# Kernel optimization log

Measured on AMD Instinct MI355X. Metric: run time of the kernel, lower is better.

Reference implementation:

```python
import jax, jax.numpy as jnp
import numpy as np

H = 51  # hidden size hardcoded in the module
B, T, FUT = 4096, 512, 16


def setup_inputs() -> dict:
    key = jax.random.key(0)
    ks = jax.random.split(key, 12)
    s = 1.0 / np.sqrt(H)  # PyTorch default uniform init bound
    u = lambda k, shape: jax.random.uniform(k, shape, jnp.float32, -s, s)
    return {
        "input": jax.random.normal(ks[0], (B, T), jnp.float32),
        "W_ih1": u(ks[1], (4 * H, 1)),
        "W_hh1": u(ks[2], (4 * H, H)),
        "b_ih1": u(ks[3], (4 * H,)),
        "b_hh1": u(ks[4], (4 * H,)),
        "W_ih2": u(ks[5], (4 * H, H)),
        "W_hh2": u(ks[6], (4 * H, H)),
        "b_ih2": u(ks[7], (4 * H,)),
        "b_hh2": u(ks[8], (4 * H,)),
        "W_lin": u(ks[9], (1, H)),
        "b_lin": u(ks[10], (1,)),
        "future": FUT,
    }


def _cell(x, h, c, Wih, Whh, b):
    # PyTorch LSTMCell gate order: i, f, g, o
    g = x @ Wih.T + h @ Whh.T + b
    i, f, gg, o = jnp.split(g, 4, axis=-1)
    c = jax.nn.sigmoid(f) * c + jax.nn.sigmoid(i) * jnp.tanh(gg)
    h = jax.nn.sigmoid(o) * jnp.tanh(c)
    return h, c


def _forward(input, W_ih1, W_hh1, b_ih1, b_hh1, W_ih2, W_hh2, b_ih2, b_hh2, W_lin, b_lin, future):
    bsz = input.shape[0]
    dt = input.dtype
    b1 = b_ih1 + b_hh1
    b2 = b_ih2 + b_hh2
    z = jnp.zeros((bsz, H), dt)
    init = (z, z, z, z)

    def step(carry, x_t):
        h1, c1, h2, c2 = carry
        h1, c1 = _cell(x_t[:, None], h1, c1, W_ih1, W_hh1, b1)
        h2, c2 = _cell(h1, h2, c2, W_ih2, W_hh2, b2)
        out = h2 @ W_lin.T + b_lin  # [b, 1]
        return (h1, c1, h2, c2), out

    (h1, c1, h2, c2), outs = jax.lax.scan(step, init, input.T)  # outs: [t, b, 1]

    def fstep(carry, _):
        h1, c1, h2, c2, out = carry
        h1, c1 = _cell(out, h1, c1, W_ih1, W_hh1, b1)
        h2, c2 = _cell(h1, h2, c2, W_ih2, W_hh2, b2)
        out = h2 @ W_lin.T + b_lin
        return (h1, c1, h2, c2, out), out

    _, fouts = jax.lax.scan(fstep, (h1, c1, h2, c2, outs[-1]), None, length=future)
    all_outs = jnp.concatenate([outs, fouts], axis=0)  # [t+future, b, 1]
    return all_outs[..., 0].T  # [b, t+future]


def reference(input, W_ih1, W_hh1, b_ih1, b_hh1, W_ih2, W_hh2, b_ih2, b_hh2, W_lin, b_lin, future):
    return _forward(input, W_ih1, W_hh1, b_ih1, b_hh1, W_ih2, W_hh2, b_ih2, b_hh2, W_lin, b_lin, future)
```

## Files before the change

kernel.cpp:

```cpp
#include <hip/hip_runtime.h>

#define TSEQ 512
#define FUT  16
#define OT   (TSEQ + FUT)
#define NB   16
#define NWAVE 13
#define NTHREADS (NWAVE * 64)
#define OBS  20

typedef _Float16 f16x8 __attribute__((ext_vector_type(8)));
typedef float    f32x4 __attribute__((ext_vector_type(4)));

#define NL2E  (-1.44269504089f)
#define N2L2E (-2.88539008178f)

__device__ __forceinline__ f32x4 mfma16(f16x8 a, f16x8 b, f32x4 c) {
    return __builtin_amdgcn_mfma_f32_16x16x32_f16(a, b, c, 0, 0, 0);
}

__device__ __forceinline__ float exp2fast(float x) {
#if __has_builtin(__builtin_amdgcn_exp2f)
    return __builtin_amdgcn_exp2f(x);
#else
    float r;
    asm("v_exp_f32 %0, %1\n\ts_nop 1" : "=v"(r) : "v"(x));
    return r;
#endif
}

__device__ __forceinline__ float cell2(const f32x4 acc, float& c) {
    const float Ei = exp2fast(acc[0]);
    const float Ef = exp2fast(acc[1]);
    const float Eg = exp2fast(acc[2]);
    const float Eo = exp2fast(acc[3]);
    const float sf   = __builtin_amdgcn_rcpf(1.0f + Ef);
    const float sitg = (1.0f - Eg) * __builtin_amdgcn_rcpf((1.0f + Ei) * (1.0f + Eg));
    c = fmaf(sf, c, sitg);
    const float Ec = exp2fast(c * N2L2E);
    return (1.0f - Ec) * __builtin_amdgcn_rcpf((1.0f + Eo) * (1.0f + Ec));
}

__global__ __launch_bounds__(NTHREADS, 1) void lstm_mfma_kernel(
    const float* __restrict__ input,
    const float* __restrict__ W_ih1,
    const float* __restrict__ W_hh1,
    const float* __restrict__ b_ih1,
    const float* __restrict__ b_hh1,
    const float* __restrict__ W_ih2,
    const float* __restrict__ W_hh2,
    const float* __restrict__ b_ih2,
    const float* __restrict__ b_hh2,
    const float* __restrict__ W_lin,
    const float* __restrict__ b_lin,
    float* __restrict__ out)
{
    const int tid  = threadIdx.x;
    const int w    = tid >> 6;
    const int lane = tid & 63;
    const int n    = lane & 15;
    const int q    = lane >> 4;
    const int b0   = blockIdx.x * NB;

    __shared__ _Float16 H1[2][2][64][8] __attribute__((aligned(16)));
    __shared__ _Float16 H2[2][2][64][8] __attribute__((aligned(16)));
    __shared__ float OB[2][16][OBS] __attribute__((aligned(16)));

    const int ru  = 4 * w + (n >> 2);
    const bool rv = (ru < 51);
    const int R   = 51 * (n & 3) + (rv ? ru : 50);
    const bool olin_row = (w == 12) && (n == 12);
    const float rsc = ((n & 3) == 2) ? N2L2E : NL2E;

    f16x8 W1h[2], W1l[2], W2h[4], W2l[4];
#pragma unroll
    for (int s = 0; s < 2; ++s) {
#pragma unroll
        for (int e = 0; e < 8; ++e) {
            const int k = 32 * s + 8 * q + e;
            float wv = 0.0f;
            if (rv) {
                if (k < 51)       wv = rsc * W_hh1[R * 51 + k];
                else if (k == 51) wv = rsc * W_ih1[R];
            }
            const _Float16 hi = (_Float16)wv;
            W1h[s][e] = hi;
            W1l[s][e] = (_Float16)(wv - (float)hi);
        }
    }
#pragma unroll
    for (int s = 0; s < 4; ++s) {
#pragma unroll
        for (int e = 0; e < 8; ++e) {
            const int k = 32 * s + 8 * q + e;
            float wv = 0.0f;
            if (rv) {
                if (k < 51)                  wv = rsc * W_ih2[R * 51 + k];
                else if (k >= 64 && k < 115) wv = rsc * W_hh2[R * 51 + (k - 64)];
            } else if (olin_row) {
                if (k >= 64 && k < 115)      wv = W_lin[k - 64];
            }
            const _Float16 hi = (_Float16)wv;
            W2h[s][e] = hi;
            W2l[s][e] = (_Float16)(wv - (float)hi);
        }
    }

    const int uu = 4 * w + q;
    const bool ustore = (uu < 51);
    const bool oduty = (w == 12) && (q == 3);
    f32x4 bias1v, bias2v;
#pragma unroll
    for (int r = 0; r < 4; ++r) {
        const int row = 51 * r + (ustore ? uu : 50);
        const float s = (r == 2) ? N2L2E : NL2E;
        bias1v[r] = ustore ? s * (b_ih1[row] + b_hh1[row]) : 0.0f;
        bias2v[r] = ustore ? s * (b_ih2[row] + b_hh2[row]) : 0.0f;
    }
    const float blin = b_lin[0];
    if (oduty) bias2v[0] = blin;
    const float wlin = ustore ? W_lin[uu] : 0.0f;
    const int uuX = ustore ? uu : 60;
    const int us = uuX >> 5;
    const int lp = n + 16 * ((uuX & 31) >> 3);
    const int ue = uuX & 7;

    {
        const f16x8 zz = {0, 0, 0, 0, 0, 0, 0, 0};
        f16x8* p1 = (f16x8*)&H1[0][0][0][0];
        f16x8* p2 = (f16x8*)&H2[0][0][0][0];
        for (int i = tid; i < 2 * 2 * 64; i += NTHREADS) { p1[i] = zz; p2[i] = zz; }
    }
    __syncthreads();

    float c1 = 0.0f, c2 = 0.0f;

    f32x4 xv = {0, 0, 0, 0}, xvn = {0, 0, 0, 0};
    if (w == 12 && q == 2) {
        xv  = *(const f32x4*)&input[(b0 + n) * TSEQ + 0];
        xvn = *(const f32x4*)&input[(b0 + n) * TSEQ + 4];
    }

    f32x4 obuf = {0, 0, 0, 0};

    {
        f16x8 xk1 = {0,0,0,0,0,0,0,0};
        if (w == 12 && q == 2) {
            xk1[3] = (_Float16)xv[0];
            H1[1][1][32 + n][3] = (_Float16)xv[1];
        }
        float x0 = input[(b0 + n) * TSEQ + 0];
        f16x8 xf = {0,0,0,0,0,0,0,0};
        if (q == 2) xf[3] = (_Float16)x0;
        f32x4 a1 = mfma16(W1h[1], xf, bias1v);
        a1 = mfma16(W1l[1], xf, a1);
        const float h1n = cell2(a1, c1);
        H1[1][us][lp][ue] = (_Float16)h1n;
    }
    __syncthreads();

#define PHASE(t_, W_, ROT_, OSL_, OSTORE_, FLUSH_, LOADN_, XW_)                \
    {                                                                          \
        const int p_  = (t_) & 1;                                              \
        const int pn_ = p_ ^ 1;                                                \
        const f16x8 h1k0 = *(const f16x8*)&H1[p_][0][lane][0];                 \
        const f16x8 h1k1 = *(const f16x8*)&H1[p_][1][lane][0];                 \
        const f16x8 h2k0 = *(const f16x8*)&H2[p_][0][lane][0];                 \
        const f16x8 h2k1 = *(const f16x8*)&H2[p_][1][lane][0];                 \
        if (w == 12) {                                                         \
            if (ROT_) xv = xvn;                                                \
            if ((LOADN_) && q == 2)                                            \
                xvn = *(const f32x4*)&input[(b0 + n) * TSEQ + (t_) + 3];       \
            if ((XW_) && q == 2)                                               \
                H1[pn_][1][32 + n][3] = (_Float16)xv[W_];                      \
        }                                                                      \
        f32x4 a1 = mfma16(W1h[0], h1k0, bias1v);                               \
        a1 = mfma16(W1l[0], h1k0, a1);                                         \
        a1 = mfma16(W1h[1], h1k1, a1);                                         \
        a1 = mfma16(W1l[1], h1k1, a1);                                         \
        f32x4 a2 = mfma16(W2h[0], h1k0, bias2v);                               \
        a2 = mfma16(W2l[0], h1k0, a2);                                         \
        a2 = mfma16(W2h[1], h1k1, a2);                                         \
        a2 = mfma16(W2l[1], h1k1, a2);                                         \
        a2 = mfma16(W2h[2], h2k0, a2);                                         \
        a2 = mfma16(W2l[2], h2k0, a2);                                         \
        a2 = mfma16(W2h[3], h2k1, a2);                                         \
        a2 = mfma16(W2l[3], h2k1, a2);                                         \
        if (OSTORE_) obuf[OSL_] = a2[0];                                       \
        if ((FLUSH_) && oduty)                                                 \
            *reinterpret_cast<f32x4*>(&out[(b0 + n) * OT + (t_) - 5]) = obuf;  \
        const float h1n = cell2(a1, c1);                                       \
        const float h2n = cell2(a2, c2);                                       \
        H1[pn_][us][lp][ue] = (_Float16)h1n;                                   \
        H2[pn_][us][lp][ue] = (_Float16)h2n;                                   \
        __syncthreads();                                                       \
    }

    PHASE(  1,   2, 0,  0,  0,  0,  0,  1)
    for (int tb = 2; tb + 3 <= 505; tb += 4) {
        PHASE(tb + 0, 3, 0, 0, 1, 0, 0, 1)
        PHASE(tb + 1, 0, 1, 1, 1, 0, 0, 1)
        PHASE(tb + 2, 1, 0, 2, 1, 0, 0, 1)
        PHASE(tb + 3, 2, 0, 3, 1, 1, 1, 1)
    }
    PHASE(506, 3, 0, 0, 1, 0, 0, 1)
    PHASE(507, 0, 1, 1, 1, 0, 0, 1)
    PHASE(508, 1, 0, 2, 1, 0, 0, 1)
    PHASE(509, 2, 0, 3, 1, 1, 0, 1)
    PHASE(510, 3, 0, 0, 1, 0, 0, 1)
    PHASE(511, 0, 0, 1, 1, 0, 0, 0)
#undef PHASE

    if (oduty) {
        out[(b0 + n) * OT + 508] = obuf[0];
        out[(b0 + n) * OT + 509] = obuf[1];
    }

    for (int t = TSEQ; t < OT; ++t) {
        const int p  = t & 1;
        const int pn = p ^ 1;

        const f16x8 h1k0 = *(const f16x8*)&H1[p][0][lane][0];
        f16x8 h1k1       = *(const f16x8*)&H1[p][1][lane][0];
        const f16x8 h2k0 = *(const f16x8*)&H2[p][0][lane][0];
        const f16x8 h2k1 = *(const f16x8*)&H2[p][1][lane][0];
        f32x4 a2 = mfma16(W2h[0], h1k0, bias2v);
        a2 = mfma16(W2l[0], h1k0, a2);
        a2 = mfma16(W2h[1], h1k1, a2);
        a2 = mfma16(W2l[1], h1k1, a2);
        a2 = mfma16(W2h[2], h2k0, a2);
        a2 = mfma16(W2l[2], h2k0, a2);
        a2 = mfma16(W2h[3], h2k1, a2);
        a2 = mfma16(W2l[3], h2k1, a2);
        if (oduty && t == TSEQ) out[(b0 + n) * OT + (TSEQ - 2)] = a2[0];
        const float h2n = cell2(a2, c2);
        H2[pn][us][lp][ue] = (_Float16)h2n;
        float po = h2n * wlin;
        po += __shfl_xor(po, 16, 64);
        po += __shfl_xor(po, 32, 64);
        if (lane < 16) OB[p][lane][w] = po;
        __syncthreads();

        float xcur = 0.0f;
        if (q == 2) {
            const float* ob = &OB[p][n][0];
            const f32x4 s0 = *(const f32x4*)&ob[0];
            const f32x4 s1 = *(const f32x4*)&ob[4];
            const f32x4 s2 = *(const f32x4*)&ob[8];
            const float o = ((s0[0] + s0[1]) + (s0[2] + s0[3]))
                          + ((s1[0] + s1[1]) + (s1[2] + s1[3]))
                          + ((s2[0] + s2[1]) + (s2[2] + s2[3])) + ob[12] + blin;
            if (w == 0) out[(b0 + n) * OT + (t - 1)] = o;
            xcur = o;
        }
        if (q == 2) h1k1[3] = (_Float16)xcur;
        f32x4 a1 = mfma16(W1h[0], h1k0, bias1v);
        a1 = mfma16(W1l[0], h1k0, a1);
        a1 = mfma16(W1h[1], h1k1, a1);
        a1 = mfma16(W1l[1], h1k1, a1);
        const float h1n = cell2(a1, c1);
        H1[pn][us][lp][ue] = (_Float16)h1n;
        __syncthreads();
    }

    {
        const f16x8 h1k0 = *(const f16x8*)&H1[0][0][lane][0];
        const f16x8 h1k1 = *(const f16x8*)&H1[0][1][lane][0];
        const f16x8 h2k0 = *(const f16x8*)&H2[0][0][lane][0];
        const f16x8 h2k1 = *(const f16x8*)&H2[0][1][lane][0];
        f32x4 a2 = mfma16(W2h[0], h1k0, bias2v);
        a2 = mfma16(W2l[0], h1k0, a2);
        a2 = mfma16(W2h[1], h1k1, a2);
        a2 = mfma16(W2l[1], h1k1, a2);
        a2 = mfma16(W2h[2], h2k0, a2);
        a2 = mfma16(W2l[2], h2k0, a2);
        a2 = mfma16(W2h[3], h2k1, a2);
        a2 = mfma16(W2l[3], h2k1, a2);
        const float h2n = cell2(a2, c2);
        float po = h2n * wlin;
        po += __shfl_xor(po, 16, 64);
        po += __shfl_xor(po, 32, 64);
        if (lane < 16) OB[0][lane][w] = po;
        __syncthreads();
        if (w == 0 && lane < 16) {
            const float* ob = &OB[0][lane][0];
            const f32x4 s0 = *(const f32x4*)&ob[0];
            const f32x4 s1 = *(const f32x4*)&ob[4];
            const f32x4 s2 = *(const f32x4*)&ob[8];
            out[(b0 + lane) * OT + (OT - 1)] =
                ((s0[0] + s0[1]) + (s0[2] + s0[3])) +
                ((s1[0] + s1[1]) + (s1[2] + s1[3])) +
                ((s2[0] + s2[1]) + (s2[2] + s2[3])) + ob[12] + blin;
        }
    }
}

extern "C" void kernel_launch(void* const* d_in, const int* in_sizes, int n_in,
                              void* d_out, int out_size, void* d_ws, size_t ws_size,
                              hipStream_t stream) {
    const float* input = (const float*)d_in[0];
    const float* W_ih1 = (const float*)d_in[1];
    const float* W_hh1 = (const float*)d_in[2];
    const float* b_ih1 = (const float*)d_in[3];
    const float* b_hh1 = (const float*)d_in[4];
    const float* W_ih2 = (const float*)d_in[5];
    const float* W_hh2 = (const float*)d_in[6];
    const float* b_ih2 = (const float*)d_in[7];
    const float* b_hh2 = (const float*)d_in[8];
    const float* W_lin = (const float*)d_in[9];
    const float* b_lin = (const float*)d_in[10];

    const int bsz = in_sizes[0] / TSEQ;

    hipLaunchKernelGGL(lstm_mfma_kernel, dim3(bsz / NB), dim3(NTHREADS), 0, stream,
                       input, W_ih1, W_hh1, b_ih1, b_hh1,
                       W_ih2, W_hh2, b_ih2, b_hh2, W_lin, b_lin,
                       (float*)d_out);
}
```

Baseline: 417.5 us.

## Cut block to 7 waves, each computing two gate tiles, allow 2 blocks/CU

Reduces the workgroup from 13 to 7 waves, so six waves now compute two 4-unit gate tiles (A and B) and one computes a single tile. Launch bounds are raised to allow two blocks per CU. The aim is to cut barrier cost per step and raise occupancy so more batch blocks run at once. The trade-off is doubled register pressure for weights per wave, a longer serial MFMA chain per wave on each step, and load imbalance from the wave without a B tile.

Result: slower. 449.9 us (+7.7%).

```diff
diff --git a/kernel.cpp b/kernel.cpp
--- a/kernel.cpp
+++ b/kernel.cpp
@@ -4,7 +4,7 @@
 #define FUT  16
 #define OT   (TSEQ + FUT)
 #define NB   16
-#define NWAVE 13
+#define NWAVE 7
 #define NTHREADS (NWAVE * 64)
 #define OBS  20
 
@@ -40,7 +40,7 @@
     return (1.0f - Ec) * __builtin_amdgcn_rcpf((1.0f + Eo) * (1.0f + Ec));
 }
 
-__global__ __launch_bounds__(NTHREADS, 1) void lstm_mfma_kernel(
+__global__ __launch_bounds__(NTHREADS, 2) void lstm_mfma_kernel(
     const float* __restrict__ input,
     const float* __restrict__ W_ih1,
     const float* __restrict__ W_hh1,
@@ -61,68 +61,90 @@
     const int q    = lane >> 4;
     const int b0   = blockIdx.x * NB;
 
+    const int tA = w;
+    const int tB = w + 7;
+    const bool hasB = (w < 6);
+
     __shared__ _Float16 H1[2][2][64][8] __attribute__((aligned(16)));
     __shared__ _Float16 H2[2][2][64][8] __attribute__((aligned(16)));
     __shared__ float OB[2][16][OBS] __attribute__((aligned(16)));
 
-    const int ru  = 4 * w + (n >> 2);
-    const bool rv = (ru < 51);
-    const int R   = 51 * (n & 3) + (rv ? ru : 50);
-    const bool olin_row = (w == 12) && (n == 12);
     const float rsc = ((n & 3) == 2) ? N2L2E : NL2E;
 
-    f16x8 W1h[2], W1l[2], W2h[4], W2l[4];
-#pragma unroll
-    for (int s = 0; s < 2; ++s) {
-#pragma unroll
-        for (int e = 0; e < 8; ++e) {
-            const int k = 32 * s + 8 * q + e;
-            float wv = 0.0f;
-            if (rv) {
-                if (k < 51)       wv = rsc * W_hh1[R * 51 + k];
-                else if (k == 51) wv = rsc * W_ih1[R];
-            }
-            const _Float16 hi = (_Float16)wv;
-            W1h[s][e] = hi;
-            W1l[s][e] = (_Float16)(wv - (float)hi);
-        }
-    }
-#pragma unroll
-    for (int s = 0; s < 4; ++s) {
-#pragma unroll
-        for (int e = 0; e < 8; ++e) {
-            const int k = 32 * s + 8 * q + e;
-            float wv = 0.0f;
-            if (rv) {
-                if (k < 51)                  wv = rsc * W_ih2[R * 51 + k];
-                else if (k >= 64 && k < 115) wv = rsc * W_hh2[R * 51 + (k - 64)];
-            } else if (olin_row) {
-                if (k >= 64 && k < 115)      wv = W_lin[k - 64];
-            }
-            const _Float16 hi = (_Float16)wv;
-            W2h[s][e] = hi;
-            W2l[s][e] = (_Float16)(wv - (float)hi);
-        }
-    }
-
-    const int uu = 4 * w + q;
-    const bool ustore = (uu < 51);
-    const bool oduty = (w == 12) && (q == 3);
-    f32x4 bias1v, bias2v;
+    f16x8 W1hA[2], W1lA[2], W2hA[4], W2lA[4];
+    f16x8 W1hB[2], W1lB[2], W2hB[4], W2lB[4];
+
+#define LOADW(TT, W1h, W1l, W2h, W2l)                                          \
+    {                                                                          \
+        const int ru = 4 * (TT) + (n >> 2);                                    \
+        const bool rv = (ru < 51);                                             \
+        const int R = 51 * (n & 3) + (rv ? ru : 50);                           \
+        const bool olin = ((TT) == 12) && (n == 12);                           \
+        _Pragma("unroll")                                                      \
+        for (int s = 0; s < 2; ++s) {                                          \
+            _Pragma("unroll")                                                  \
+            for (int e = 0; e < 8; ++e) {                                      \
+                const int k = 32 * s + 8 * q + e;                              \
+                float wv = 0.0f;                                               \
+                if (rv) {                                                      \
+                    if (k < 51)       wv = rsc * W_hh1[R * 51 + k];            \
+                    else if (k == 51) wv = rsc * W_ih1[R];                     \
+                }                                                              \
+                const _Float16 hi = (_Float16)wv;                              \
+                W1h[s][e] = hi;                                                \
+                W1l[s][e] = (_Float16)(wv - (float)hi);                        \
+            }                                                                  \
+        }                                                                      \
+        _Pragma("unroll")                                                      \
+        for (int s = 0; s < 4; ++s) {                                          \
+            _Pragma("unroll")                                                  \
+            for (int e = 0; e < 8; ++e) {                                      \
+                const int k = 32 * s + 8 * q + e;                              \
+                float wv = 0.0f;                                               \
+                if (rv) {                                                      \
+                    if (k < 51)                  wv = rsc * W_ih2[R * 51 + k]; \
+                    else if (k >= 64 && k < 115) wv = rsc * W_hh2[R * 51 + (k - 64)]; \
+                } else if (olin) {                                             \
+                    if (k >= 64 && k < 115)      wv = W_lin[k - 64];           \
+                }                                                              \
+                const _Float16 hi = (_Float16)wv;                              \
+                W2h[s][e] = hi;                                                \
+                W2l[s][e] = (_Float16)(wv - (float)hi);                        \
+            }                                                                  \
+        }                                                                      \
+    }
+
+    LOADW(tA, W1hA, W1lA, W2hA, W2lA)
+    LOADW(tB, W1hB, W1lB, W2hB, W2lB)
+#undef LOADW
+
+    const int uuA = 4 * tA + q;
+    const int uuB = 4 * tB + q;
+    const bool ustA = (uuA < 51);
+    const bool ustB = (uuB < 51) && hasB;
+    const bool oduty = (w == 5) && (q == 3);
+    const float blin = b_lin[0];
+
+    f32x4 bias1A, bias2A, bias1B, bias2B;
 #pragma unroll
     for (int r = 0; r < 4; ++r) {
-        const int row = 51 * r + (ustore ? uu : 50);
         const float s = (r == 2) ? N2L2E : NL2E;
-        bias1v[r] = ustore ? s * (b_ih1[row] + b_hh1[row]) : 0.0f;
-        bias2v[r] = ustore ? s * (b_ih2[row] + b_hh2[row]) : 0.0f;
-    }
-    const float blin = b_lin[0];
-    if (oduty) bias2v[0] = blin;
-    const float wlin = ustore ? W_lin[uu] : 0.0f;
-    const int uuX = ustore ? uu : 60;
-    const int us = uuX >> 5;
-    const int lp = n + 16 * ((uuX & 31) >> 3);
-    const int ue = uuX & 7;
+        const int rowA = 51 * r + (ustA ? uuA : 50);
+        bias1A[r] = ustA ? s * (b_ih1[rowA] + b_hh1[rowA]) : 0.0f;
+        bias2A[r] = ustA ? s * (b_ih2[rowA] + b_hh2[rowA]) : 0.0f;
+        const int rowB = 51 * r + (ustB ? uuB : 50);
+        bias1B[r] = ustB ? s * (b_ih1[rowB] + b_hh1[rowB]) : 0.0f;
+        bias2B[r] = ustB ? s * (b_ih2[rowB] + b_hh2[rowB]) : 0.0f;
+    }
+    if (oduty) bias2B[0] = blin;
+
+    const float wlinA = ustA ? W_lin[uuA] : 0.0f;
+    const float wlinB = ustB ? W_lin[uuB] : 0.0f;
+
+    const int uuXA = ustA ? uuA : 60;
+    const int usA = uuXA >> 5, lpA = n + 16 * ((uuXA & 31) >> 3), ueA = uuXA & 7;
+    const int uuXB = ustB ? uuB : 60;
+    const int usB = uuXB >> 5, lpB = n + 16 * ((uuXB & 31) >> 3), ueB = uuXB & 7;
 
     {
         const f16x8 zz = {0, 0, 0, 0, 0, 0, 0, 0};
@@ -132,10 +154,10 @@
     }
     __syncthreads();
 
-    float c1 = 0.0f, c2 = 0.0f;
+    float c1A = 0.0f, c2A = 0.0f, c1B = 0.0f, c2B = 0.0f;
 
     f32x4 xv = {0, 0, 0, 0}, xvn = {0, 0, 0, 0};
-    if (w == 12 && q == 2) {
+    if (w == 6 && q == 2) {
         xv  = *(const f32x4*)&input[(b0 + n) * TSEQ + 0];
         xvn = *(const f32x4*)&input[(b0 + n) * TSEQ + 4];
     }
@@ -143,18 +165,20 @@
     f32x4 obuf = {0, 0, 0, 0};
 
     {
-        f16x8 xk1 = {0,0,0,0,0,0,0,0};
-        if (w == 12 && q == 2) {
-            xk1[3] = (_Float16)xv[0];
-            H1[1][1][32 + n][3] = (_Float16)xv[1];
-        }
-        float x0 = input[(b0 + n) * TSEQ + 0];
+        const float x0 = input[(b0 + n) * TSEQ + 0];
+        if (w == 6 && q == 2) H1[1][1][32 + n][3] = (_Float16)xv[1];
         f16x8 xf = {0,0,0,0,0,0,0,0};
         if (q == 2) xf[3] = (_Float16)x0;
-        f32x4 a1 = mfma16(W1h[1], xf, bias1v);
-        a1 = mfma16(W1l[1], xf, a1);
-        const float h1n = cell2(a1, c1);
-        H1[1][us][lp][ue] = (_Float16)h1n;
+        f32x4 a1 = mfma16(W1hA[1], xf, bias1A);
+        a1 = mfma16(W1lA[1], xf, a1);
+        const float h1A = cell2(a1, c1A);
+        H1[1][usA][lpA][ueA] = (_Float16)h1A;
+        if (hasB) {
+            f32x4 b1 = mfma16(W1hB[1], xf, bias1B);
+            b1 = mfma16(W1lB[1], xf, b1);
+            const float h1B = cell2(b1, c1B);
+            H1[1][usB][lpB][ueB] = (_Float16)h1B;
+        }
     }
     __syncthreads();
 
@@ -166,32 +190,50 @@
         const f16x8 h1k1 = *(const f16x8*)&H1[p_][1][lane][0];                 \
         const f16x8 h2k0 = *(const f16x8*)&H2[p_][0][lane][0];                 \
         const f16x8 h2k1 = *(const f16x8*)&H2[p_][1][lane][0];                 \
-        if (w == 12) {                                                         \
+        if (w == 6) {                                                          \
             if (ROT_) xv = xvn;                                                \
             if ((LOADN_) && q == 2)                                            \
                 xvn = *(const f32x4*)&input[(b0 + n) * TSEQ + (t_) + 3];       \
             if ((XW_) && q == 2)                                               \
                 H1[pn_][1][32 + n][3] = (_Float16)xv[W_];                      \
         }                                                                      \
-        f32x4 a1 = mfma16(W1h[0], h1k0, bias1v);                               \
-        a1 = mfma16(W1l[0], h1k0, a1);                                         \
-        a1 = mfma16(W1h[1], h1k1, a1);                                         \
-        a1 = mfma16(W1l[1], h1k1, a1);                                         \
-        f32x4 a2 = mfma16(W2h[0], h1k0, bias2v);                               \
-        a2 = mfma16(W2l[0], h1k0, a2);                                         \
-        a2 = mfma16(W2h[1], h1k1, a2);                                         \
-        a2 = mfma16(W2l[1], h1k1, a2);                                         \
-        a2 = mfma16(W2h[2], h2k0, a2);                                         \
-        a2 = mfma16(W2l[2], h2k0, a2);                                         \
-        a2 = mfma16(W2h[3], h2k1, a2);                                         \
-        a2 = mfma16(W2l[3], h2k1, a2);                                         \
-        if (OSTORE_) obuf[OSL_] = a2[0];                                       \
-        if ((FLUSH_) && oduty)                                                 \
-            *reinterpret_cast<f32x4*>(&out[(b0 + n) * OT + (t_) - 5]) = obuf;  \
-        const float h1n = cell2(a1, c1);                                       \
-        const float h2n = cell2(a2, c2);                                       \
-        H1[pn_][us][lp][ue] = (_Float16)h1n;                                   \
-        H2[pn_][us][lp][ue] = (_Float16)h2n;                                   \
+        f32x4 a1 = mfma16(W1hA[0], h1k0, bias1A);                              \
+        a1 = mfma16(W1lA[0], h1k0, a1);                                        \
+        a1 = mfma16(W1hA[1], h1k1, a1);                                        \
+        a1 = mfma16(W1lA[1], h1k1, a1);                                        \
+        f32x4 a2 = mfma16(W2hA[0], h1k0, bias2A);                              \
+        a2 = mfma16(W2lA[0], h1k0, a2);                                        \
+        a2 = mfma16(W2hA[1], h1k1, a2);                                        \
+        a2 = mfma16(W2lA[1], h1k1, a2);                                        \
+        a2 = mfma16(W2hA[2], h2k0, a2);                                        \
+        a2 = mfma16(W2lA[2], h2k0, a2);                                        \
+        a2 = mfma16(W2hA[3], h2k1, a2);                                        \
+        a2 = mfma16(W2lA[3], h2k1, a2);                                        \
+        const float h1nA = cell2(a1, c1A);                                     \
+        const float h2nA = cell2(a2, c2A);                                     \
+        H1[pn_][usA][lpA][ueA] = (_Float16)h1nA;                               \
+        H2[pn_][usA][lpA][ueA] = (_Float16)h2nA;                               \
+        if (hasB) {                                                            \
+            f32x4 b1 = mfma16(W1hB[0], h1k0, bias1B);                          \
+            b1 = mfma16(W1lB[0], h1k0, b1);                                    \
+            b1 = mfma16(W1hB[1], h1k1, b1);                                    \
+            b1 = mfma16(W1lB[1], h1k1, b1);                                    \
+            f32x4 b2 = mfma16(W2hB[0], h1k0, bias2B);                          \
+            b2 = mfma16(W2lB[0], h1k0, b2);                                    \
+            b2 = mfma16(W2hB[1], h1k1, b2);                                    \
+            b2 = mfma16(W2lB[1], h1k1, b2);                                    \
+            b2 = mfma16(W2hB[2], h2k0, b2);                                    \
+            b2 = mfma16(W2lB[2], h2k0, b2);                                    \
+            b2 = mfma16(W2hB[3], h2k1, b2);                                    \
+            b2 = mfma16(W2lB[3], h2k1, b2);                                    \
+            if (OSTORE_) obuf[OSL_] = b2[0];                                   \
+            if ((FLUSH_) && oduty)                                             \
+                *reinterpret_cast<f32x4*>(&out[(b0 + n) * OT + (t_) - 5]) = obuf; \
+            const float h1nB = cell2(b1, c1B);                                 \
+            const float h2nB = cell2(b2, c2B);                                 \
+            H1[pn_][usB][lpB][ueB] = (_Float16)h1nB;                           \
+            H2[pn_][usB][lpB][ueB] = (_Float16)h2nB;                           \
+        }                                                                      \
         __syncthreads();                                                       \
     }
 
@@ -223,21 +265,37 @@
         f16x8 h1k1       = *(const f16x8*)&H1[p][1][lane][0];
         const f16x8 h2k0 = *(const f16x8*)&H2[p][0][lane][0];
         const f16x8 h2k1 = *(const f16x8*)&H2[p][1][lane][0];
-        f32x4 a2 = mfma16(W2h[0], h1k0, bias2v);
-        a2 = mfma16(W2l[0], h1k0, a2);
-        a2 = mfma16(W2h[1], h1k1, a2);
-        a2 = mfma16(W2l[1], h1k1, a2);
-        a2 = mfma16(W2h[2], h2k0, a2);
-        a2 = mfma16(W2l[2], h2k0, a2);
-        a2 = mfma16(W2h[3], h2k1, a2);
-        a2 = mfma16(W2l[3], h2k1, a2);
-        if (oduty && t == TSEQ) out[(b0 + n) * OT + (TSEQ - 2)] = a2[0];
-        const float h2n = cell2(a2, c2);
-        H2[pn][us][lp][ue] = (_Float16)h2n;
-        float po = h2n * wlin;
-        po += __shfl_xor(po, 16, 64);
-        po += __shfl_xor(po, 32, 64);
-        if (lane < 16) OB[p][lane][w] = po;
+        f32x4 a2 = mfma16(W2hA[0], h1k0, bias2A);
+        a2 = mfma16(W2lA[0], h1k0, a2);
+        a2 = mfma16(W2hA[1], h1k1, a2);
+        a2 = mfma16(W2lA[1], h1k1, a2);
+        a2 = mfma16(W2hA[2], h2k0, a2);
+        a2 = mfma16(W2lA[2], h2k0, a2);
+        a2 = mfma16(W2hA[3], h2k1, a2);
+        a2 = mfma16(W2lA[3], h2k1, a2);
+        const float h2nA = cell2(a2, c2A);
+        H2[pn][usA][lpA][ueA] = (_Float16)h2nA;
+        float poA = h2nA * wlinA;
+        poA += __shfl_xor(poA, 16, 64);
+        poA += __shfl_xor(poA, 32, 64);
+        if (lane < 16) OB[p][lane][tA] = poA;
+        if (hasB) {
+            f32x4 b2 = mfma16(W2hB[0], h1k0, bias2B);
+            b2 = mfma16(W2lB[0], h1k0, b2);
+            b2 = mfma16(W2hB[1], h1k1, b2);
+            b2 = mfma16(W2lB[1], h1k1, b2);
+            b2 = mfma16(W2hB[2], h2k0, b2);
+            b2 = mfma16(W2lB[2], h2k0, b2);
+            b2 = mfma16(W2hB[3], h2k1, b2);
+            b2 = mfma16(W2lB[3], h2k1, b2);
+            if (oduty && t == TSEQ) out[(b0 + n) * OT + (TSEQ - 2)] = b2[0];
+            const float h2nB = cell2(b2, c2B);
+            H2[pn][usB][lpB][ueB] = (_Float16)h2nB;
+            float poB = h2nB * wlinB;
+            poB += __shfl_xor(poB, 16, 64);
+            poB += __shfl_xor(poB, 32, 64);
+            if (lane < 16) OB[p][lane][tB] = poB;
+        }
         __syncthreads();
 
         float xcur = 0.0f;
@@ -253,12 +311,20 @@
             xcur = o;
         }
         if (q == 2) h1k1[3] = (_Float16)xcur;
-        f32x4 a1 = mfma16(W1h[0], h1k0, bias1v);
-        a1 = mfma16(W1l[0], h1k0, a1);
-        a1 = mfma16(W1h[1], h1k1, a1);
-        a1 = mfma16(W1l[1], h1k1, a1);
-        const float h1n = cell2(a1, c1);
-        H1[pn][us][lp][ue] = (_Float16)h1n;
+        f32x4 a1 = mfma16(W1hA[0], h1k0, bias1A);
+        a1 = mfma16(W1lA[0], h1k0, a1);
+        a1 = mfma16(W1hA[1], h1k1, a1);
+        a1 = mfma16(W1lA[1], h1k1, a1);
+        const float h1nA = cell2(a1, c1A);
+        H1[pn][usA][lpA][ueA] = (_Float16)h1nA;
+        if (hasB) {
+            f32x4 b1 = mfma16(W1hB[0], h1k0, bias1B);
+            b1 = mfma16(W1lB[0], h1k0, b1);
+            b1 = mfma16(W1hB[1], h1k1, b1);
+            b1 = mfma16(W1lB[1], h1k1, b1);
+            const float h1nB = cell2(b1, c1B);
+            H1[pn][usB][lpB][ueB] = (_Float16)h1nB;
+        }
         __syncthreads();
     }
 
@@ -267,19 +333,34 @@
         const f16x8 h1k1 = *(const f16x8*)&H1[0][1][lane][0];
         const f16x8 h2k0 = *(const f16x8*)&H2[0][0][lane][0];
         const f16x8 h2k1 = *(const f16x8*)&H2[0][1][lane][0];
-        f32x4 a2 = mfma16(W2h[0], h1k0, bias2v);
-        a2 = mfma16(W2l[0], h1k0, a2);
-        a2 = mfma16(W2h[1], h1k1, a2);
-        a2 = mfma16(W2l[1], h1k1, a2);
-        a2 = mfma16(W2h[2], h2k0, a2);
-        a2 = mfma16(W2l[2], h2k0, a2);
-        a2 = mfma16(W2h[3], h2k1, a2);
-        a2 = mfma16(W2l[3], h2k1, a2);
-        const float h2n = cell2(a2, c2);
-        float po = h2n * wlin;
-        po += __shfl_xor(po, 16, 64);
-        po += __shfl_xor(po, 32, 64);
-        if (lane < 16) OB[0][lane][w] = po;
+        f32x4 a2 = mfma16(W2hA[0], h1k0, bias2A);
+        a2 = mfma16(W2lA[0], h1k0, a2);
+        a2 = mfma16(W2hA[1], h1k1, a2);
+        a2 = mfma16(W2lA[1], h1k1, a2);
+        a2 = mfma16(W2hA[2], h2k0, a2);
+        a2 = mfma16(W2lA[2], h2k0, a2);
+        a2 = mfma16(W2hA[3], h2k1, a2);
+        a2 = mfma16(W2lA[3], h2k1, a2);
+        const float h2nA = cell2(a2, c2A);
+        float poA = h2nA * wlinA;
+        poA += __shfl_xor(poA, 16, 64);
+        poA += __shfl_xor(poA, 32, 64);
+        if (lane < 16) OB[0][lane][tA] = poA;
+        if (hasB) {
+            f32x4 b2 = mfma16(W2hB[0], h1k0, bias2B);
+            b2 = mfma16(W2lB[0], h1k0, b2);
+            b2 = mfma16(W2hB[1], h1k1, b2);
+            b2 = mfma16(W2lB[1], h1k1, b2);
+            b2 = mfma16(W2hB[2], h2k0, b2);
+            b2 = mfma16(W2lB[2], h2k0, b2);
+            b2 = mfma16(W2hB[3], h2k1, b2);
+            b2 = mfma16(W2lB[3], h2k1, b2);
+            const float h2nB = cell2(b2, c2B);
+            float poB = h2nB * wlinB;
+            poB += __shfl_xor(poB, 16, 64);
+            poB += __shfl_xor(poB, 32, 64);
+            if (lane < 16) OB[0][lane][tB] = poB;
+        }
         __syncthreads();
         if (w == 0 && lane < 16) {
             const float* ob = &OB[0][lane][0];
```
